# Optimization experiments

Measured on AMD Instinct MI355X. Metric: run time of the kernel, lower is better.

The kernel has to match this reference:

```python
import jax, jax.numpy as jnp
import numpy as np

B, H, T, D = 2, 16, 2048, 64
R1, R2 = 4, 8


def setup_inputs() -> dict:
    key = jax.random.key(0)
    ks = jax.random.split(key, 7)
    return {
        "q": jax.random.normal(ks[0], (B, H, T, D), dtype=jnp.float32),
        "k": jax.random.normal(ks[1], (B, H, T, D), dtype=jnp.float32),
        "v": jax.random.normal(ks[2], (B, H, T, D), dtype=jnp.float32),
        "W_q": jax.random.normal(ks[3], (H, D, R1 * R2), dtype=jnp.float32) / np.sqrt(D),
        "W_k": jax.random.normal(ks[4], (H, D, R1 * R2), dtype=jnp.float32) / np.sqrt(D),
        "core1": jax.random.normal(ks[5], (H, R1), dtype=jnp.float32),
        "core2": jax.random.normal(ks[6], (H, R2), dtype=jnp.float32),
    }


def reference(q, k, v, W_q, W_k, core1, core2):
    """Kronecker low-rank (LSR) causal attention.

    scores[b,h,m,n] = (1/sqrt(R1*R2)) * sum_r kron[h,r] * (q@W_q)[b,h,m,r] * (k@W_k)[b,h,n,r]
    where kron[h] = core1[h] (x) core2[h]  (per-head Kronecker product).
    """
    Hh, r1 = core1.shape
    r2 = core2.shape[1]
    # per-head Kronecker core vector: (H, R1*R2)
    kron = (core1[:, :, None] * core2[:, None, :]).reshape(Hh, r1 * r2)
    scale = 1.0 / jnp.sqrt(jnp.float32(r1 * r2))
    # low-rank projections, rank R = R1*R2
    q_lr = jnp.einsum("bhtd,hdr->bhtr", q, W_q) * kron[None, :, None, :]  # [B,H,T,R]
    k_lr = jnp.einsum("bhtd,hdr->bhtr", k, W_k)                            # [B,H,T,R]
    scores = jnp.einsum("bhmr,bhnr->bhmn", q_lr, k_lr) * scale             # [B,H,T,T]
    t = q.shape[2]
    causal = jnp.tril(jnp.ones((t, t), dtype=bool))
    scores = jnp.where(causal[None, None], scores, -jnp.inf)
    p = jax.nn.softmax(scores, axis=-1)
    return jnp.einsum("bhmn,bhnd->bhmd", p, v)
```

## Files before the change

### kernel.cpp

```cpp
#include <hip/hip_runtime.h>

typedef _Float16 f16;
typedef _Float16 f16x2 __attribute__((ext_vector_type(2)));
typedef _Float16 f16x4 __attribute__((ext_vector_type(4)));
typedef _Float16 f16x8 __attribute__((ext_vector_type(8)));
typedef float    f32x4 __attribute__((ext_vector_type(4)));
typedef float    f32x16 __attribute__((ext_vector_type(16)));

constexpr int B_ = 2, H_ = 16, T_ = 2048, D_ = 64, R_ = 32, NT = 32;
constexpr int NROW = B_ * H_ * T_;

__device__ __forceinline__ f32x4 mfma16(f16x8 a, f16x8 b, f32x4 c) {
  return __builtin_amdgcn_mfma_f32_16x16x32_f16(a, b, c, 0, 0, 0);
}
__device__ __forceinline__ f32x16 mfma32(f16x8 a, f16x8 b, f32x16 c) {
  return __builtin_amdgcn_mfma_f32_32x32x16_f16(a, b, c, 0, 0, 0);
}
__device__ __forceinline__ void ld_lds16(const void* g, void* l) {
  __builtin_amdgcn_global_load_lds(
      (const __attribute__((address_space(1))) unsigned int*)g,
      (__attribute__((address_space(3))) unsigned int*)l, 16, 0, 0);
}

__global__ __launch_bounds__(256) void proj_kernel(
    const float* __restrict__ q, const float* __restrict__ k, const float* __restrict__ v,
    const float* __restrict__ Wq, const float* __restrict__ Wk,
    const float* __restrict__ c1, const float* __restrict__ c2,
    f16* __restrict__ qlr, f16* __restrict__ klr, f16* __restrict__ vt)
{
  __shared__ float sv[64 * 65];

  const int tid = threadIdx.x, w = tid >> 6, lane = tid & 63;
  const int l15 = lane & 15, l4 = lane >> 4;
  const int bh = blockIdx.x >> 5, h = bh & (H_ - 1);
  const int t0 = (blockIdx.x & 31) * 64;

  const float* vb = v + ((size_t)bh * T_ + t0) * D_;
  float4 vld[4];
#pragma unroll
  for (int it = 0; it < 4; ++it) vld[it] = ((const float4*)vb)[it * 256 + tid];

  const int m = t0 + 16 * w + l15;
  const float* qr = q + ((size_t)bh * T_ + m) * D_;
  const float* kr = k + ((size_t)bh * T_ + m) * D_;
  f16x8 aq[2], ak[2];
#pragma unroll
  for (int kc = 0; kc < 2; ++kc) {
    float4 x0 = *(const float4*)(qr + kc * 32 + 8 * l4);
    float4 x1 = *(const float4*)(qr + kc * 32 + 8 * l4 + 4);
    float4 y0 = *(const float4*)(kr + kc * 32 + 8 * l4);
    float4 y1 = *(const float4*)(kr + kc * 32 + 8 * l4 + 4);
    f16x8 A, K;
    A[0]=(f16)x0.x; A[1]=(f16)x0.y; A[2]=(f16)x0.z; A[3]=(f16)x0.w;
    A[4]=(f16)x1.x; A[5]=(f16)x1.y; A[6]=(f16)x1.z; A[7]=(f16)x1.w;
    K[0]=(f16)y0.x; K[1]=(f16)y0.y; K[2]=(f16)y0.z; K[3]=(f16)y0.w;
    K[4]=(f16)y1.x; K[5]=(f16)y1.y; K[6]=(f16)y1.z; K[7]=(f16)y1.w;
    aq[kc] = A; ak[kc] = K;
  }

  const float* Wqh = Wq + (size_t)h * D_ * R_;
  const float* Wkh = Wk + (size_t)h * D_ * R_;
  f16x8 bq[2][2], bk[2][2];
#pragma unroll
  for (int kc = 0; kc < 2; ++kc)
#pragma unroll
    for (int nt = 0; nt < 2; ++nt) {
      const int r = 16 * nt + l15;
      f16x8 q8, k8;
#pragma unroll
      for (int j2 = 0; j2 < 8; ++j2) {
        const int d = kc * 32 + 8 * l4 + j2;
        q8[j2] = (f16)Wqh[d * R_ + r];
        k8[j2] = (f16)Wkh[d * R_ + r];
      }
      bq[kc][nt] = q8; bk[kc][nt] = k8;
    }

#pragma unroll
  for (int it = 0; it < 4; ++it) {
    const int i4 = it * 256 + tid, t = i4 >> 4, dq = (i4 & 15) * 4;
    sv[t * 65 + dq    ] = vld[it].x;
    sv[t * 65 + dq + 1] = vld[it].y;
    sv[t * 65 + dq + 2] = vld[it].z;
    sv[t * 65 + dq + 3] = vld[it].w;
  }

  const f32x4 z4 = {0.f, 0.f, 0.f, 0.f};
#pragma unroll
  for (int nt = 0; nt < 2; ++nt) {
    f32x4 accq = mfma16(aq[0], bq[0][nt], z4);
    accq = mfma16(aq[1], bq[1][nt], accq);
    f32x4 acck = mfma16(ak[0], bk[0][nt], z4);
    acck = mfma16(ak[1], bk[1][nt], acck);
    const int r = 16 * nt + l15;
    const float scl = c1[h * 4 + (r >> 3)] * c2[h * 8 + (r & 7)] *
                      (0.17677669529663687f * 1.4426950408889634f);
#pragma unroll
    for (int i = 0; i < 4; ++i) {
      const size_t row = (size_t)bh * T_ + t0 + 16 * w + 4 * l4 + i;
      qlr[row * R_ + r] = (f16)(accq[i] * scl);
      klr[row * R_ + r] = (f16)acck[i];
    }
  }

  __syncthreads();
#pragma unroll
  for (int it = 0; it < 8; ++it) {
    const int idx = it * 256 + tid, d = idx >> 5, t = (idx & 31) * 2;
    const float f0 = sv[t * 65 + d], f1 = sv[t * 65 + 65 + d];
    f16x2 pr; pr[0] = (f16)f0; pr[1] = (f16)f1;
    const int sw = ((((t >> 3) ^ (d & 7)) << 3) | (t & 7));
    *(f16x2*)(vt + ((size_t)bh * D_ + d) * T_ + t0 + sw) = pr;
  }
}

__global__ __launch_bounds__(128) void attn_kernel(
    const f16* __restrict__ qlr, const f16* __restrict__ klr,
    const f16* __restrict__ vt, f16* __restrict__ On, float2* __restrict__ ml,
    const int NS)
{
  __shared__ __align__(16) f16 s_k[64 * 32];
  __shared__ __align__(16) f16 s_vt[64 * 64];
  __shared__ __align__(16) f16 s_p[2][32 * 64];

  const int tid = threadIdx.x, w = tid >> 6, lane = tid & 63;
  const int l15 = lane & 15, l4 = lane >> 4, l31 = lane & 31, hh = lane >> 5;
  const int bh = blockIdx.x & 31;
  const int rest = blockIdx.x >> 5;
  const int mt = 31 - ((NS == 2) ? (rest >> 1) : rest);
  const int s  = rest & (NS - 1);
  const int m0 = mt * 64;

  const f16x8 aq0 = *(const f16x8*)(qlr + ((size_t)bh * T_ + m0 + 32 * w + l15) * R_ + 8 * l4);
  const f16x8 aq1 = *(const f16x8*)(qlr + ((size_t)bh * T_ + m0 + 32 * w + 16 + l15) * R_ + 8 * l4);

  const f16* kb = klr + (size_t)bh * T_ * R_;
  const f16* vb = vt + (size_t)bh * D_ * T_;

  f32x16 oacc[2];
#pragma unroll
  for (int c = 0; c < 2; ++c)
#pragma unroll
    for (int e = 0; e < 16; ++e) oacc[c][e] = 0.f;
  float mi0 = -1e30f, mi1 = -1e30f, li0 = 0.f, li1 = 0.f;
  const f32x4 z4 = {0.f, 0.f, 0.f, 0.f};

  for (int j = s; j <= mt; j += NS) {
    const int n0 = 64 * j;
    __syncthreads();
#pragma unroll
    for (int e = 0; e < 2; ++e)
      ld_lds16((const char*)kb + (size_t)n0 * 64 + (2 * w + e) * 1024 + lane * 16,
               (char*)s_k + (2 * w + e) * 1024);
#pragma unroll
    for (int e = 0; e < 4; ++e) {
      const int d0 = w * 32 + e * 8;
      ld_lds16((const char*)vb + ((size_t)(d0 + (lane >> 3)) * T_ + n0) * 2 + (lane & 7) * 16,
               (char*)s_vt + d0 * 128);
    }
    __syncthreads();

    f32x4 sc[4][2];
#pragma unroll
    for (int ns = 0; ns < 4; ++ns) {
      f16x8 akf = *(const f16x8*)&s_k[(16 * ns + l15) * 32 + 8 * l4];
      sc[ns][0] = mfma16(akf, aq0, z4);
      sc[ns][1] = mfma16(akf, aq1, z4);
    }
    if (j == mt) {
      const int lim0 = 32 * w + l15;
#pragma unroll
      for (int ns = 0; ns < 4; ++ns) {
        const int nb = 16 * ns + 4 * l4;
#pragma unroll
        for (int i = 0; i < 4; ++i) {
          if (nb + i > lim0)      sc[ns][0][i] = -1e30f;
          if (nb + i > lim0 + 16) sc[ns][1][i] = -1e30f;
        }
      }
    }

    float rm0 = -1e30f, rm1 = -1e30f;
#pragma unroll
    for (int ns = 0; ns < 4; ++ns)
#pragma unroll
      for (int i = 0; i < 4; ++i) {
        rm0 = fmaxf(rm0, sc[ns][0][i]);
        rm1 = fmaxf(rm1, sc[ns][1][i]);
      }
    rm0 = fmaxf(rm0, __shfl_xor(rm0, 16)); rm0 = fmaxf(rm0, __shfl_xor(rm0, 32));
    rm1 = fmaxf(rm1, __shfl_xor(rm1, 16)); rm1 = fmaxf(rm1, __shfl_xor(rm1, 32));
    const float mn0 = fmaxf(mi0, rm0), mn1 = fmaxf(mi1, rm1);
    const float a0 = exp2f(mi0 - mn0), a1 = exp2f(mi1 - mn1);
    float rs0 = 0.f, rs1 = 0.f;
#pragma unroll
    for (int ns = 0; ns < 4; ++ns) {
      f16x4 p0v, p1v;
#pragma unroll
      for (int i = 0; i < 4; ++i) {
        const float p0 = exp2f(sc[ns][0][i] - mn0);
        const float p1 = exp2f(sc[ns][1][i] - mn1);
        rs0 += p0; rs1 += p1;
        p0v[i] = (f16)p0; p1v[i] = (f16)p1;
      }
      const int col = ((((2 * ns + (l4 >> 1)) ^ (l15 & 7)) << 3) | (4 * (l4 & 1)));
      *(f16x4*)&s_p[w][l15 * 64 + col]        = p0v;
      *(f16x4*)&s_p[w][(16 + l15) * 64 + col] = p1v;
    }
    rs0 += __shfl_xor(rs0, 16); rs0 += __shfl_xor(rs0, 32);
    rs1 += __shfl_xor(rs1, 16); rs1 += __shfl_xor(rs1, 32);
    li0 = li0 * a0 + rs0; li1 = li1 * a1 + rs1;
    mi0 = mn0; mi1 = mn1;
    const float aPV = (lane & 16) ? a1 : a0;
#pragma unroll
    for (int c = 0; c < 2; ++c) oacc[c] *= aPV;

#pragma unroll
    for (int kc = 0; kc < 4; ++kc) {
      const int u = (2 * kc + hh) ^ (l31 & 7);
      f16x8 bp = *(const f16x8*)&s_p[w][l31 * 64 + u * 8];
#pragma unroll
      for (int c = 0; c < 2; ++c) {
        f16x8 av = *(const f16x8*)&s_vt[(32 * c + l31) * 64 + u * 8];
        oacc[c] = mfma32(av, bp, oacc[c]);
      }
    }
  }

  const float myl = (lane & 16) ? li1 : li0;
  const float invl = myl > 0.f ? 1.f / myl : 0.f;
  f16* ob = On + (((size_t)s * 32 + bh) * T_ + m0 + 32 * w + l31) * D_;
#pragma unroll
  for (int c = 0; c < 2; ++c)
#pragma unroll
    for (int g = 0; g < 4; ++g) {
      f16x4 o;
#pragma unroll
      for (int e = 0; e < 4; ++e) o[e] = (f16)(oacc[c][4 * g + e] * invl);
      *(f16x4*)(ob + 32 * c + 8 * g + 4 * hh) = o;
    }
  if (l4 < 2) {
    float2 mlv;
    mlv.x = l4 ? mi1 : mi0;
    mlv.y = l4 ? li1 : li0;
    ml[((size_t)s * 32 + bh) * T_ + m0 + 32 * w + 16 * l4 + l15] = mlv;
  }
}

__global__ __launch_bounds__(256) void merge_kernel(
    const f16* __restrict__ On, const float2* __restrict__ ml,
    float* __restrict__ out, const int NS)
{
  const int row = blockIdx.x * 32 + (threadIdx.x >> 3);
  const int d0 = (threadIdx.x & 7) * 8;
  const f16x8 o0 = *(const f16x8*)(On + (size_t)row * 64 + d0);
  float res[8];
  if (NS == 2) {
    const float2 a = ml[row];
    const float2 b = ml[NROW + row];
    const f16x8 o1 = *(const f16x8*)(On + ((size_t)NROW + row) * 64 + d0);
    const float ms = fmaxf(a.x, b.x);
    const float w0 = exp2f(a.x - ms) * a.y;
    const float w1 = exp2f(b.x - ms) * b.y;
    const float inv = 1.f / (w0 + w1);
    const float c0 = w0 * inv, c1 = w1 * inv;
#pragma unroll
    for (int e = 0; e < 8; ++e) res[e] = c0 * (float)o0[e] + c1 * (float)o1[e];
  } else {
#pragma unroll
    for (int e = 0; e < 8; ++e) res[e] = (float)o0[e];
  }
  float* ob = out + (size_t)row * 64 + d0;
  f32x4 r0, r1;
#pragma unroll
  for (int e = 0; e < 4; ++e) { r0[e] = res[e]; r1[e] = res[4 + e]; }
  *(f32x4*)ob = r0;
  *(f32x4*)(ob + 4) = r1;
}

extern "C" void kernel_launch(void* const* d_in, const int* in_sizes, int n_in,
                              void* d_out, int out_size, void* d_ws, size_t ws_size,
                              hipStream_t stream) {
  const float* q  = (const float*)d_in[0];
  const float* k  = (const float*)d_in[1];
  const float* v  = (const float*)d_in[2];
  const float* Wq = (const float*)d_in[3];
  const float* Wk = (const float*)d_in[4];
  const float* c1 = (const float*)d_in[5];
  const float* c2 = (const float*)d_in[6];
  float* out = (float*)d_out;

  f16* qlr = (f16*)d_ws;
  f16* klr = qlr + (size_t)B_ * H_ * T_ * R_;
  f16* vt  = klr + (size_t)B_ * H_ * T_ * R_;
  f16* On  = vt + (size_t)B_ * H_ * T_ * D_;
  float2* ml = (float2*)(On + (size_t)2 * NROW * D_);

  const int NS = (ws_size >= ((size_t)33 * 1024 * 1024 + (1 << 20))) ? 2 : 1;

  proj_kernel<<<B_ * H_ * NT, 256, 0, stream>>>(q, k, v, Wq, Wk, c1, c2, qlr, klr, vt);
  attn_kernel<<<B_ * H_ * NT * NS, 128, 0, stream>>>(qlr, klr, vt, On, ml, NS);
  merge_kernel<<<NROW / 32, 256, 0, stream>>>(On, ml, out, NS);
}
```

Baseline: 153.7 us.

## Allow four-way KV split and stage projection weights and outputs through LDS

The attention kernel can now split the key range into up to four parts instead of two when the workspace is large enough, with a generalized merge that combines NS partial results by their log-sum-exp weights. The projection kernel now loads W_q/W_k coalesced into shared memory instead of doing strided per-lane global reads, stages qlr/klr outputs in LDS so they are written as 16-byte vectors, and stores V in LDS as fp16. The wider split aims to improve occupancy and load balance for the causal tiles, at the cost of more partial-output traffic and merge work.

Result: slower. 167.4 us (+8.9%).

```diff
diff --git a/kernel.cpp b/kernel.cpp
--- a/kernel.cpp
+++ b/kernel.cpp
@@ -28,7 +28,9 @@
     const float* __restrict__ c1, const float* __restrict__ c2,
     f16* __restrict__ qlr, f16* __restrict__ klr, f16* __restrict__ vt)
 {
-  __shared__ float sv[64 * 65];
+  __shared__ f16   sv[64 * 65];
+  __shared__ float sW[2][64 * 33];
+  __shared__ f16   sO[2][64 * 40];
 
   const int tid = threadIdx.x, w = tid >> 6, lane = tid & 63;
   const int l15 = lane & 15, l4 = lane >> 4;
@@ -57,58 +59,66 @@
     K[4]=(f16)y1.x; K[5]=(f16)y1.y; K[6]=(f16)y1.z; K[7]=(f16)y1.w;
     aq[kc] = A; ak[kc] = K;
   }
-
   const float* Wqh = Wq + (size_t)h * D_ * R_;
   const float* Wkh = Wk + (size_t)h * D_ * R_;
-  f16x8 bq[2][2], bk[2][2];
-#pragma unroll
-  for (int kc = 0; kc < 2; ++kc)
-#pragma unroll
-    for (int nt = 0; nt < 2; ++nt) {
-      const int r = 16 * nt + l15;
-      f16x8 q8, k8;
+  float4 wq0 = ((const float4*)Wqh)[tid * 2], wq1 = ((const float4*)Wqh)[tid * 2 + 1];
+  float4 wk0 = ((const float4*)Wkh)[tid * 2], wk1 = ((const float4*)Wkh)[tid * 2 + 1];
+
+#pragma unroll
+  for (int it = 0; it < 4; ++it) {
+    const int i4 = it * 256 + tid, t = i4 >> 4, dq = (i4 & 15) * 4;
+    sv[t * 65 + dq    ] = (f16)vld[it].x;
+    sv[t * 65 + dq + 1] = (f16)vld[it].y;
+    sv[t * 65 + dq + 2] = (f16)vld[it].z;
+    sv[t * 65 + dq + 3] = (f16)vld[it].w;
+  }
+  {
+    const int d = tid >> 2, r0 = (tid & 3) * 8;
+    float* pq = &sW[0][d * 33 + r0];
+    float* pk = &sW[1][d * 33 + r0];
+    pq[0]=wq0.x; pq[1]=wq0.y; pq[2]=wq0.z; pq[3]=wq0.w;
+    pq[4]=wq1.x; pq[5]=wq1.y; pq[6]=wq1.z; pq[7]=wq1.w;
+    pk[0]=wk0.x; pk[1]=wk0.y; pk[2]=wk0.z; pk[3]=wk0.w;
+    pk[4]=wk1.x; pk[5]=wk1.y; pk[6]=wk1.z; pk[7]=wk1.w;
+  }
+  __syncthreads();
+
+  const f32x4 z4 = {0.f, 0.f, 0.f, 0.f};
+#pragma unroll
+  for (int nt = 0; nt < 2; ++nt) {
+    const int r = 16 * nt + l15;
+    f16x8 bq[2], bk[2];
+#pragma unroll
+    for (int kc = 0; kc < 2; ++kc)
 #pragma unroll
       for (int j2 = 0; j2 < 8; ++j2) {
         const int d = kc * 32 + 8 * l4 + j2;
-        q8[j2] = (f16)Wqh[d * R_ + r];
-        k8[j2] = (f16)Wkh[d * R_ + r];
-      }
-      bq[kc][nt] = q8; bk[kc][nt] = k8;
-    }
-
-#pragma unroll
-  for (int it = 0; it < 4; ++it) {
-    const int i4 = it * 256 + tid, t = i4 >> 4, dq = (i4 & 15) * 4;
-    sv[t * 65 + dq    ] = vld[it].x;
-    sv[t * 65 + dq + 1] = vld[it].y;
-    sv[t * 65 + dq + 2] = vld[it].z;
-    sv[t * 65 + dq + 3] = vld[it].w;
-  }
-
-  const f32x4 z4 = {0.f, 0.f, 0.f, 0.f};
-#pragma unroll
-  for (int nt = 0; nt < 2; ++nt) {
-    f32x4 accq = mfma16(aq[0], bq[0][nt], z4);
-    accq = mfma16(aq[1], bq[1][nt], accq);
-    f32x4 acck = mfma16(ak[0], bk[0][nt], z4);
-    acck = mfma16(ak[1], bk[1][nt], acck);
-    const int r = 16 * nt + l15;
+        bq[kc][j2] = (f16)sW[0][d * 33 + r];
+        bk[kc][j2] = (f16)sW[1][d * 33 + r];
+      }
+    f32x4 accq = mfma16(aq[0], bq[0], z4); accq = mfma16(aq[1], bq[1], accq);
+    f32x4 acck = mfma16(ak[0], bk[0], z4); acck = mfma16(ak[1], bk[1], acck);
     const float scl = c1[h * 4 + (r >> 3)] * c2[h * 8 + (r & 7)] *
                       (0.17677669529663687f * 1.4426950408889634f);
 #pragma unroll
     for (int i = 0; i < 4; ++i) {
-      const size_t row = (size_t)bh * T_ + t0 + 16 * w + 4 * l4 + i;
-      qlr[row * R_ + r] = (f16)(accq[i] * scl);
-      klr[row * R_ + r] = (f16)acck[i];
-    }
-  }
-
+      const int row = 16 * w + 4 * l4 + i;
+      sO[0][row * 40 + r] = (f16)(accq[i] * scl);
+      sO[1][row * 40 + r] = (f16)acck[i];
+    }
+  }
   __syncthreads();
+
+  {
+    const int row = tid >> 2, seg = (tid & 3) * 8;
+    const size_t g = ((size_t)bh * T_ + t0 + row) * R_ + seg;
+    *(f16x8*)(qlr + g) = *(const f16x8*)&sO[0][row * 40 + seg];
+    *(f16x8*)(klr + g) = *(const f16x8*)&sO[1][row * 40 + seg];
+  }
 #pragma unroll
   for (int it = 0; it < 8; ++it) {
     const int idx = it * 256 + tid, d = idx >> 5, t = (idx & 31) * 2;
-    const float f0 = sv[t * 65 + d], f1 = sv[t * 65 + 65 + d];
-    f16x2 pr; pr[0] = (f16)f0; pr[1] = (f16)f1;
+    f16x2 pr; pr[0] = sv[t * 65 + d]; pr[1] = sv[(t + 1) * 65 + d];
     const int sw = ((((t >> 3) ^ (d & 7)) << 3) | (t & 7));
     *(f16x2*)(vt + ((size_t)bh * D_ + d) * T_ + t0 + sw) = pr;
   }
@@ -117,7 +127,7 @@
 __global__ __launch_bounds__(128) void attn_kernel(
     const f16* __restrict__ qlr, const f16* __restrict__ klr,
     const f16* __restrict__ vt, f16* __restrict__ On, float2* __restrict__ ml,
-    const int NS)
+    const int ns_shift)
 {
   __shared__ __align__(16) f16 s_k[64 * 32];
   __shared__ __align__(16) f16 s_vt[64 * 64];
@@ -125,9 +135,10 @@
 
   const int tid = threadIdx.x, w = tid >> 6, lane = tid & 63;
   const int l15 = lane & 15, l4 = lane >> 4, l31 = lane & 31, hh = lane >> 5;
+  const int NS = 1 << ns_shift;
   const int bh = blockIdx.x & 31;
   const int rest = blockIdx.x >> 5;
-  const int mt = 31 - ((NS == 2) ? (rest >> 1) : rest);
+  const int mt = 31 - (rest >> ns_shift);
   const int s  = rest & (NS - 1);
   const int m0 = mt * 64;
 
@@ -253,22 +264,32 @@
 {
   const int row = blockIdx.x * 32 + (threadIdx.x >> 3);
   const int d0 = (threadIdx.x & 7) * 8;
-  const f16x8 o0 = *(const f16x8*)(On + (size_t)row * 64 + d0);
   float res[8];
-  if (NS == 2) {
-    const float2 a = ml[row];
-    const float2 b = ml[NROW + row];
-    const f16x8 o1 = *(const f16x8*)(On + ((size_t)NROW + row) * 64 + d0);
-    const float ms = fmaxf(a.x, b.x);
-    const float w0 = exp2f(a.x - ms) * a.y;
-    const float w1 = exp2f(b.x - ms) * b.y;
-    const float inv = 1.f / (w0 + w1);
-    const float c0 = w0 * inv, c1 = w1 * inv;
-#pragma unroll
-    for (int e = 0; e < 8; ++e) res[e] = c0 * (float)o0[e] + c1 * (float)o1[e];
+  if (NS == 1) {
+    const f16x8 o0 = *(const f16x8*)(On + (size_t)row * 64 + d0);
+#pragma unroll
+    for (int e = 0; e < 8; ++e) res[e] = (float)o0[e];
   } else {
-#pragma unroll
-    for (int e = 0; e < 8; ++e) res[e] = (float)o0[e];
+    float2 mls[4];
+    float ms = -3e38f;
+    for (int s = 0; s < NS; ++s) {
+      mls[s] = ml[(size_t)s * NROW + row];
+      ms = fmaxf(ms, mls[s].x);
+    }
+    float wt[4], wsum = 0.f;
+    for (int s = 0; s < NS; ++s) {
+      wt[s] = exp2f(mls[s].x - ms) * mls[s].y;
+      wsum += wt[s];
+    }
+    const float inv = 1.f / wsum;
+#pragma unroll
+    for (int e = 0; e < 8; ++e) res[e] = 0.f;
+    for (int s = 0; s < NS; ++s) {
+      const f16x8 o = *(const f16x8*)(On + ((size_t)s * NROW + row) * 64 + d0);
+      const float c = wt[s] * inv;
+#pragma unroll
+      for (int e = 0; e < 8; ++e) res[e] += c * (float)o[e];
+    }
   }
   float* ob = out + (size_t)row * 64 + d0;
   f32x4 r0, r1;
@@ -294,11 +315,16 @@
   f16* klr = qlr + (size_t)B_ * H_ * T_ * R_;
   f16* vt  = klr + (size_t)B_ * H_ * T_ * R_;
   f16* On  = vt + (size_t)B_ * H_ * T_ * D_;
-  float2* ml = (float2*)(On + (size_t)2 * NROW * D_);
-
-  const int NS = (ws_size >= ((size_t)33 * 1024 * 1024 + (1 << 20))) ? 2 : 1;
+
+  const size_t projB = (size_t)16 * 1024 * 1024;
+  const size_t perSplit = (size_t)NROW * D_ * 2 + (size_t)NROW * 8;
+  int ns_shift = 0;
+  if (ws_size >= projB + 4 * perSplit) ns_shift = 2;
+  else if (ws_size >= projB + 2 * perSplit) ns_shift = 1;
+  const int NS = 1 << ns_shift;
+  float2* ml = (float2*)(On + (size_t)NS * NROW * D_);
 
   proj_kernel<<<B_ * H_ * NT, 256, 0, stream>>>(q, k, v, Wq, Wk, c1, c2, qlr, klr, vt);
-  attn_kernel<<<B_ * H_ * NT * NS, 128, 0, stream>>>(qlr, klr, vt, On, ml, NS);
+  attn_kernel<<<B_ * H_ * NT * NS, 128, 0, stream>>>(qlr, klr, vt, On, ml, ns_shift);
   merge_kernel<<<NROW / 32, 256, 0, stream>>>(On, ml, out, NS);
 }
```
